# Kernel tuning notes

Measured on AMD Instinct MI355X. Metric: run time of the kernel, lower is better.

## Reference

```python
import jax, jax.numpy as jnp
import numpy as np


def setup_inputs() -> dict:
    key = jax.random.key(0)
    k1, k2, k3 = jax.random.split(key, 3)
    B, D, F = 4096, 1024, 16384  # batch, input_dim, dict_size
    x = jax.random.normal(k1, (B, D), dtype=jnp.float32)
    W_enc = jax.random.normal(k2, (F, D), dtype=jnp.float32) * (1.0 / np.sqrt(D))
    b_enc = jnp.zeros((F,), dtype=jnp.float32)
    W_dec = jax.random.normal(k3, (D, F), dtype=jnp.float32)
    # decoder columns are unit-normalized (as in _normalize_decoder)
    W_dec = W_dec / jnp.clip(jnp.linalg.norm(W_dec, axis=0, keepdims=True), 1e-8)
    b_dec = jnp.zeros((D,), dtype=jnp.float32)
    return {"x": x, "W_enc": W_enc, "b_enc": b_enc, "W_dec": W_dec, "b_dec": b_dec, "k": 32}


def reference(x, W_enc, b_enc, W_dec, b_dec, k):
    # encode: z_pre = (x - b_dec) @ W_enc^T + b_enc   -> [B, F]
    x_centered = x - b_dec
    z_pre = jnp.einsum('bd,fd->bf', x_centered, W_enc) + b_enc
    # activate: TopK(ReLU(z_pre)) via top_k + relu + scatter
    topk_vals, topk_idx = jax.lax.top_k(z_pre, k)           # [B, k]
    B = z_pre.shape[0]
    rows = jnp.arange(B)[:, None]                            # [B, 1]
    z = jnp.zeros_like(z_pre).at[rows, topk_idx].set(jax.nn.relu(topk_vals))
    # decode: x_hat = z @ W_dec^T + b_dec (dense matmul over sparse z)
    x_hat = jnp.einsum('bf,df->bd', z, W_dec) + b_dec
    return (x_hat, z, z_pre)
```

## Files before the change

kernel.cpp:

```cpp
#include <hip/hip_runtime.h>
#include <cstdint>
#include <cfloat>
#include <cstddef>

#define MAXK 128

typedef __attribute__((ext_vector_type(8))) short bf16x8;
typedef __attribute__((ext_vector_type(4))) float f32x4;

__device__ __forceinline__ void split8(const float4& v0, const float4& v1,
                                       uint4& hp, uint4& lp)
{
    float vv[8] = {v0.x, v0.y, v0.z, v0.w, v1.x, v1.y, v1.z, v1.w};
    unsigned h[8], l[8];
    #pragma unroll
    for (int i = 0; i < 8; ++i) {
        unsigned u  = __float_as_uint(vv[i]);
        unsigned hb = u & 0xFFFF0000u;
        float lf    = vv[i] - __uint_as_float(hb);
        h[i] = u;
        l[i] = __float_as_uint(lf);
    }
    hp.x = (h[0] >> 16) | (h[1] & 0xFFFF0000u);
    hp.y = (h[2] >> 16) | (h[3] & 0xFFFF0000u);
    hp.z = (h[4] >> 16) | (h[5] & 0xFFFF0000u);
    hp.w = (h[6] >> 16) | (h[7] & 0xFFFF0000u);
    lp.x = (l[0] >> 16) | (l[1] & 0xFFFF0000u);
    lp.y = (l[2] >> 16) | (l[3] & 0xFFFF0000u);
    lp.z = (l[4] >> 16) | (l[5] & 0xFFFF0000u);
    lp.w = (l[6] >> 16) | (l[7] & 0xFFFF0000u);
}

__device__ __forceinline__ void gload_lds16(const void* g, void* l)
{
    __builtin_amdgcn_global_load_lds(
        (const __attribute__((address_space(1))) unsigned int*)g,
        (__attribute__((address_space(3))) unsigned int*)l,
        16, 0, 0);
}

__global__ __launch_bounds__(256)
void prep_x_kernel(const float* __restrict__ x, const float* __restrict__ b_dec,
                   ushort* __restrict__ AhiP, ushort* __restrict__ AloP, int D)
{
    const int c   = blockIdx.x * 256 + threadIdx.x;
    const int t   = c >> 9;
    const int wc  = c & 511;
    const int rl  = wc >> 2;
    const int pkc = wc & 3;
    const int kc  = (pkc - (rl >> 1)) & 3;
    const int nkb = D >> 5;
    const int band = t / nkb, kblk = t - band * nkb;
    const int row = band * 128 + rl;
    const int k0  = kblk * 32 + kc * 8;

    const float* src = x + (size_t)row * D + k0;
    float4 v0 = *(const float4*)(src);
    float4 v1 = *(const float4*)(src + 4);
    const float* bd = b_dec + k0;
    float4 d0 = *(const float4*)(bd);
    float4 d1 = *(const float4*)(bd + 4);
    v0.x -= d0.x; v0.y -= d0.y; v0.z -= d0.z; v0.w -= d0.w;
    v1.x -= d1.x; v1.y -= d1.y; v1.z -= d1.z; v1.w -= d1.w;
    uint4 hp, lp;
    split8(v0, v1, hp, lp);
    const size_t off = (size_t)t * 4096 + (size_t)wc * 8;
    *(uint4*)&AhiP[off] = hp;
    *(uint4*)&AloP[off] = lp;
}

__global__ __launch_bounds__(256)
void prep_w_kernel(const float* __restrict__ Wenc,
                   ushort* __restrict__ WhiP, ushort* __restrict__ WloP, int D)
{
    const int c   = blockIdx.x * 256 + threadIdx.x;
    const int t   = c >> 10;
    const int wc  = c & 1023;
    const int rl  = wc >> 2;
    const int pkc = wc & 3;
    const int kc  = (pkc - (rl >> 1)) & 3;
    const int nkb = D >> 5;
    const int fband = t / nkb, kblk = t - fband * nkb;
    const int f   = fband * 256 + rl;
    const int k0  = kblk * 32 + kc * 8;

    const float* src = Wenc + (size_t)f * D + k0;
    float4 v0 = *(const float4*)(src);
    float4 v1 = *(const float4*)(src + 4);
    uint4 hp, lp;
    split8(v0, v1, hp, lp);
    const size_t off = (size_t)t * 8192 + (size_t)wc * 8;
    *(uint4*)&WhiP[off] = hp;
    *(uint4*)&WloP[off] = lp;
}

__global__ __launch_bounds__(256, 2)
void encode_gemm_pre(const ushort* __restrict__ AhiP, const ushort* __restrict__ AloP,
                     const ushort* __restrict__ WhiP, const ushort* __restrict__ WloP,
                     const float* __restrict__ b_enc, float* __restrict__ z_pre,
                     int D, int F)
{
    __shared__ ushort AsHi[4096];
    __shared__ ushort AsLo[4096];
    __shared__ ushort BsHi[2][8192];
    __shared__ ushort BsLo[2][8192];

    const int tid = threadIdx.x;
    const int bm  = blockIdx.y * 128;
    const int bn  = blockIdx.x * 256;

    const int lane = tid & 63;
    const int w    = tid >> 6;
    const int wm   = (w >> 1) * 64;
    const int wn   = (w & 1) * 128;
    const int fr   = lane & 15;
    const int q    = lane >> 4;
    const int nkb  = D >> 5;

    int aoff[4], boff[8];
    #pragma unroll
    for (int mi = 0; mi < 4; ++mi) {
        const int r = wm + mi * 16 + fr;
        aoff[mi] = r * 32 + (((q + (r >> 1)) & 3) * 8);
    }
    #pragma unroll
    for (int ni = 0; ni < 8; ++ni) {
        const int r = wn + ni * 16 + fr;
        boff[ni] = r * 32 + (((q + (r >> 1)) & 3) * 8);
    }

    f32x4 acc[4][8];
    #pragma unroll
    for (int mi = 0; mi < 4; ++mi)
        #pragma unroll
        for (int ni = 0; ni < 8; ++ni)
            acc[mi][ni] = (f32x4){0.f, 0.f, 0.f, 0.f};

    const char* aHi = (const char*)AhiP + (size_t)blockIdx.y * nkb * 8192;
    const char* aLo = (const char*)AloP + (size_t)blockIdx.y * nkb * 8192;
    const char* bHi = (const char*)WhiP + (size_t)blockIdx.x * nkb * 16384;
    const char* bLo = (const char*)WloP + (size_t)blockIdx.x * nkb * 16384;
    const int la16 = lane * 16;

    auto stageA = [&](int kb) {
        const char* pa = aHi + (size_t)kb * 8192;
        const char* pl = aLo + (size_t)kb * 8192;
        #pragma unroll
        for (int c = 0; c < 2; ++c) {
            const int off = (w * 2 + c) * 1024;
            gload_lds16(pa + off + la16, (char*)AsHi + off);
            gload_lds16(pl + off + la16, (char*)AsLo + off);
        }
    };
    auto stageB = [&](int kb, int buf) {
        const char* pb = bHi + (size_t)kb * 16384;
        const char* pm = bLo + (size_t)kb * 16384;
        #pragma unroll
        for (int c = 0; c < 4; ++c) {
            const int off = (w * 4 + c) * 1024;
            gload_lds16(pb + off + la16, (char*)&BsHi[buf][0] + off);
            gload_lds16(pm + off + la16, (char*)&BsLo[buf][0] + off);
        }
    };

    stageA(0);
    stageB(0, 0);
    asm volatile("s_waitcnt vmcnt(0)" ::: "memory");
    __syncthreads();

    int cur = 0;
    for (int kb = 0; kb < nkb; ++kb) {
        bf16x8 ahi[4], alo[4];
        #pragma unroll
        for (int mi = 0; mi < 4; ++mi) {
            ahi[mi] = *(const bf16x8*)&AsHi[aoff[mi]];
            alo[mi] = *(const bf16x8*)&AsLo[aoff[mi]];
        }
        __syncthreads();
        if (kb + 1 < nkb) {
            stageA(kb + 1);
            stageB(kb + 1, cur ^ 1);
        }
        const ushort* sBH = &BsHi[cur][0];
        const ushort* sBL = &BsLo[cur][0];
        #pragma unroll
        for (int ni = 0; ni < 8; ++ni) {
            bf16x8 bhi = *(const bf16x8*)&sBH[boff[ni]];
            bf16x8 blo = *(const bf16x8*)&sBL[boff[ni]];
            #pragma unroll
            for (int mi = 0; mi < 4; ++mi) {
                acc[mi][ni] = __builtin_amdgcn_mfma_f32_16x16x32_bf16(alo[mi], bhi, acc[mi][ni], 0, 0, 0);
                acc[mi][ni] = __builtin_amdgcn_mfma_f32_16x16x32_bf16(ahi[mi], blo, acc[mi][ni], 0, 0, 0);
                acc[mi][ni] = __builtin_amdgcn_mfma_f32_16x16x32_bf16(ahi[mi], bhi, acc[mi][ni], 0, 0, 0);
            }
        }
        asm volatile("s_waitcnt vmcnt(0)" ::: "memory");
        __syncthreads();
        cur ^= 1;
    }

    #pragma unroll
    for (int ni = 0; ni < 8; ++ni) {
        const int col = bn + wn + ni * 16 + fr;
        const float be = b_enc[col];
        #pragma unroll
        for (int mi = 0; mi < 4; ++mi) {
            const int rbase = bm + wm + mi * 16 + q * 4;
            float* dst = z_pre + (size_t)rbase * F + col;
            #pragma unroll
            for (int r = 0; r < 4; ++r)
                dst[(size_t)r * F] = acc[mi][ni][r] + be;
        }
    }
}

__global__ __launch_bounds__(256, 2)
void encode_gemm_bf16x3(const float* __restrict__ x, const float* __restrict__ Wenc,
                        const float* __restrict__ b_enc, const float* __restrict__ b_dec,
                        float* __restrict__ z_pre, int D, int F)
{
    constexpr int BM = 128, BN = 256, BK = 32;
    __shared__ ushort AsHi[BM * BK];
    __shared__ ushort AsLo[BM * BK];
    __shared__ ushort BsHi[BN * BK];
    __shared__ ushort BsLo[BN * BK];

    const int tid = threadIdx.x;
    const int bm  = blockIdx.y * BM;
    const int bn  = blockIdx.x * BN;

    const int lane = tid & 63;
    const int w    = tid >> 6;
    const int wm   = (w >> 1) * 64;
    const int wn   = (w & 1) * 128;
    const int fr   = lane & 15;
    const int q    = lane >> 4;

    int aoff[4], boff[8];
    #pragma unroll
    for (int mi = 0; mi < 4; ++mi) {
        const int r = wm + mi * 16 + fr;
        aoff[mi] = r * 32 + (((q + (r >> 1)) & 3) * 8);
    }
    #pragma unroll
    for (int ni = 0; ni < 8; ++ni) {
        const int r = wn + ni * 16 + fr;
        boff[ni] = r * 32 + (((q + (r >> 1)) & 3) * 8);
    }

    f32x4 acc[4][8];
    #pragma unroll
    for (int mi = 0; mi < 4; ++mi)
        #pragma unroll
        for (int ni = 0; ni < 8; ++ni)
            acc[mi][ni] = (f32x4){0.f, 0.f, 0.f, 0.f};

    for (int k0 = 0; k0 < D; k0 += BK) {
        #pragma unroll
        for (int j = 0; j < 2; ++j) {
            const int task = tid + 256 * j;
            const int row = task >> 2, kc = task & 3;
            const float* src = x + (size_t)(bm + row) * D + k0 + kc * 8;
            float4 v0 = *(const float4*)(src);
            float4 v1 = *(const float4*)(src + 4);
            const float* bd = b_dec + k0 + kc * 8;
            float4 d0 = *(const float4*)(bd);
            float4 d1 = *(const float4*)(bd + 4);
            v0.x -= d0.x; v0.y -= d0.y; v0.z -= d0.z; v0.w -= d0.w;
            v1.x -= d1.x; v1.y -= d1.y; v1.z -= d1.z; v1.w -= d1.w;
            uint4 hp, lp;
            split8(v0, v1, hp, lp);
            const int off = row * 32 + (((kc + (row >> 1)) & 3) * 8);
            *(uint4*)&AsHi[off] = hp;
            *(uint4*)&AsLo[off] = lp;
        }
        #pragma unroll
        for (int j = 0; j < 4; ++j) {
            const int task = tid + 256 * j;
            const int row = task >> 2, kc = task & 3;
            const float* src = Wenc + (size_t)(bn + row) * D + k0 + kc * 8;
            float4 v0 = *(const float4*)(src);
            float4 v1 = *(const float4*)(src + 4);
            uint4 hp, lp;
            split8(v0, v1, hp, lp);
            const int off = row * 32 + (((kc + (row >> 1)) & 3) * 8);
            *(uint4*)&BsHi[off] = hp;
            *(uint4*)&BsLo[off] = lp;
        }
        __syncthreads();

        bf16x8 ahi[4], alo[4];
        #pragma unroll
        for (int mi = 0; mi < 4; ++mi) {
            ahi[mi] = *(const bf16x8*)&AsHi[aoff[mi]];
            alo[mi] = *(const bf16x8*)&AsLo[aoff[mi]];
        }
        #pragma unroll
        for (int ni = 0; ni < 8; ++ni) {
            bf16x8 bhi = *(const bf16x8*)&BsHi[boff[ni]];
            bf16x8 blo = *(const bf16x8*)&BsLo[boff[ni]];
            #pragma unroll
            for (int mi = 0; mi < 4; ++mi) {
                acc[mi][ni] = __builtin_amdgcn_mfma_f32_16x16x32_bf16(alo[mi], bhi, acc[mi][ni], 0, 0, 0);
                acc[mi][ni] = __builtin_amdgcn_mfma_f32_16x16x32_bf16(ahi[mi], blo, acc[mi][ni], 0, 0, 0);
                acc[mi][ni] = __builtin_amdgcn_mfma_f32_16x16x32_bf16(ahi[mi], bhi, acc[mi][ni], 0, 0, 0);
            }
        }
        __syncthreads();
    }

    #pragma unroll
    for (int ni = 0; ni < 8; ++ni) {
        const int col = bn + wn + ni * 16 + fr;
        const float be = b_enc[col];
        #pragma unroll
        for (int mi = 0; mi < 4; ++mi) {
            const int rbase = bm + wm + mi * 16 + q * 4;
            float* dst = z_pre + (size_t)rbase * F + col;
            #pragma unroll
            for (int r = 0; r < 4; ++r)
                dst[(size_t)r * F] = acc[mi][ni][r] + be;
        }
    }
}

__device__ __forceinline__ unsigned fkey(float f)
{
    unsigned u = __float_as_uint(f);
    return u ^ ((unsigned)((int)u >> 31) | 0x80000000u);
}
__device__ __forceinline__ float finv(unsigned k)
{
    unsigned u = (k & 0x80000000u) ? (k ^ 0x80000000u) : ~k;
    return __uint_as_float(u);
}

__device__ __forceinline__ float exact_zpre(const float* __restrict__ xr,
                                            const float* __restrict__ Wenc,
                                            const float* __restrict__ b_enc,
                                            const float* __restrict__ b_dec,
                                            int f, int D, int ln)
{
    const float* wr = Wenc + (size_t)f * D;
    float s = 0.f;
    for (int d = ln * 4; d < D; d += 256) {
        float4 xv = *(const float4*)(xr + d);
        float4 bd = *(const float4*)(b_dec + d);
        float4 wv4 = *(const float4*)(wr + d);
        s = fmaf(xv.x - bd.x, wv4.x, s);
        s = fmaf(xv.y - bd.y, wv4.y, s);
        s = fmaf(xv.z - bd.z, wv4.z, s);
        s = fmaf(xv.w - bd.w, wv4.w, s);
    }
    #pragma unroll
    for (int o = 32; o > 0; o >>= 1) s += __shfl_down(s, o, 64);
    return s + b_enc[f];
}

#define DLT 4e-3f

template <int NVEC>
__global__ __launch_bounds__(256)
void topk_fast(const float* __restrict__ z_pre, float* __restrict__ z,
               float* __restrict__ ws_vals, int* __restrict__ ws_idx,
               const int* __restrict__ k_ptr,
               const float* __restrict__ x, const float* __restrict__ Wenc,
               const float* __restrict__ b_enc, const float* __restrict__ b_dec,
               int F, int D)
{
    const int row = blockIdx.x;
    const int t   = threadIdx.x;
    const int k   = *k_ptr;
    const int nv4 = F >> 2;
    const int wv_id = t >> 6, ln = t & 63;

    __shared__ ushort keys[16384];
    __shared__ float  cand_v[256];
    __shared__ int    cand_i[256];
    __shared__ unsigned char cand_sel[256];
    __shared__ int    bnd[128];
    __shared__ float  s2w[4];
    __shared__ int    hist4[4][256];
    __shared__ int    waveTot[4];
    __shared__ int    s_bin, s_above;
    __shared__ int    n_c_s, n_b_s, c_hi_s, out_cnt, cnt_tau_s, bad_s;
    __shared__ unsigned vk_key;

    if (t == 0) {
        n_c_s = 0; n_b_s = 0; c_hi_s = 0; out_cnt = 0; cnt_tau_s = 0; bad_s = 0;
        vk_key = 0xFFFFFFFFu;
    }

    const float*  zrow = z_pre + (size_t)row * F;
    const float4* src  = (const float4*)zrow;
    float4* dstz = (float4*)(z + (size_t)row * F);
    const float4 zz = make_float4(0.f, 0.f, 0.f, 0.f);

    float s2 = 0.f;
    #pragma unroll
    for (int i = 0; i < NVEC; ++i) {
        const int p = t + 256 * i;
        if (p < nv4) {
            const float4 v = src[p];
            dstz[p] = zz;
            const unsigned k0 = fkey(v.x) >> 16;
            const unsigned k1 = fkey(v.y) >> 16;
            const unsigned k2 = fkey(v.z) >> 16;
            const unsigned k3 = fkey(v.w) >> 16;
            uint2 pk;
            pk.x = k0 | (k1 << 16);
            pk.y = k2 | (k3 << 16);
            *(uint2*)&keys[p * 4] = pk;
            s2 = fmaf(v.x, v.x, s2);
            s2 = fmaf(v.y, v.y, s2);
            s2 = fmaf(v.z, v.z, s2);
            s2 = fmaf(v.w, v.w, s2);
        }
    }
    #pragma unroll
    for (int o = 32; o > 0; o >>= 1) s2 += __shfl_down(s2, o, 64);
    if (ln == 0) s2w[wv_id] = s2;
    __syncthreads();

    const float sigma = sqrtf((s2w[0] + s2w[1] + s2w[2] + s2w[3]) / (float)F);
    int c0 = 4 * k; if (c0 < 64) c0 = 64; if (c0 > 192) c0 = 192;
    const float qq  = (float)c0 / (float)F;
    const float tt  = sqrtf(-2.f * logf(qq));
    const float phi = tt - (2.30753f + 0.27061f * tt) /
                           (1.f + 0.99229f * tt + 0.04481f * tt * tt);
    const float tau = sigma * phi;
    const unsigned tk = fkey(tau) >> 16;
    const unsigned tkey16 = (tk >= 2) ? (tk - 2) : 0;

    const int nU = nv4 * 2;
    const unsigned* keysU = (const unsigned*)keys;
    for (int j = t; j < nU; j += 256) {
        const unsigned pr = keysU[j];
        const unsigned ka = pr & 0xFFFFu, kb = pr >> 16;
        if (ka > tkey16) { const int s = atomicAdd(&n_c_s, 1); if (s < 256) cand_i[s] = 2 * j; }
        if (kb > tkey16) { const int s = atomicAdd(&n_c_s, 1); if (s < 256) cand_i[s] = 2 * j + 1; }
    }
    __syncthreads();

    if (t == 0 && (n_c_s > 256 || !(tau > 0.1f))) bad_s = 1;
    const int n_c = min(n_c_s, 256);

    float myv = 0.f;
    if (t < n_c) {
        myv = zrow[cand_i[t]];
        cand_v[t] = myv;
        if (myv > tau) atomicAdd(&cnt_tau_s, 1);
    }
    __syncthreads();
    if (t == 0 && cnt_tau_s < k) bad_s = 1;

    cand_sel[t] = 0;
    if (t < n_c) {
        int gt = 0;
        for (int j = 0; j < n_c; ++j) gt += (cand_v[j] > myv);
        if (gt <= k - 1) atomicMin(&vk_key, fkey(myv));
    }
    __syncthreads();

    const float vkv = finv(vk_key);
    if (t < n_c) {
        if (myv > vkv + DLT) {
            cand_sel[t] = 2;
            atomicAdd(&c_hi_s, 1);
        } else if (myv > vkv - DLT) {
            const int sb = atomicAdd(&n_b_s, 1);
            if (sb < 128) bnd[sb] = t;
        }
    }
    __syncthreads();
    if (t == 0 && n_b_s > 128) bad_s = 1;
    __syncthreads();

    if (!bad_s) {
        const int n_b = n_b_s;
        const float* xr = x + (size_t)row * D;
        for (int b2 = wv_id; b2 < n_b; b2 += 4) {
            const int c = bnd[b2];
            const float ex = exact_zpre(xr, Wenc, b_enc, b_dec, cand_i[c], D, ln);
            if (ln == 0) cand_v[c] = ex;
        }
        __syncthreads();

        if (t == 0) {
            int need = k - c_hi_s;
            if (need > n_b) need = n_b;
            for (int it = 0; it < need; ++it) {
                int bi = -1; float bv = 0.f;
                for (int b2 = 0; b2 < n_b; ++b2) {
                    const int c = bnd[b2];
                    if (cand_sel[c]) continue;
                    const float v = cand_v[c];
                    if (bi < 0 || v > bv || (v == bv && cand_i[c] < cand_i[bi])) {
                        bi = c; bv = v;
                    }
                }
                if (bi < 0) break;
                cand_sel[bi] = 1;
            }
        }
        __syncthreads();

        float* wvp = ws_vals + (size_t)row * MAXK;
        int*   wip = ws_idx  + (size_t)row * MAXK;
        if (t < n_c && cand_sel[t]) {
            const float zv = fmaxf(cand_v[t], 0.f);
            z[(size_t)row * F + cand_i[t]] = zv;
            const int s = atomicAdd(&out_cnt, 1);
            if (s < MAXK) { wvp[s] = zv; wip[s] = cand_i[t]; }
        }
        return;
    }

    if (t == 0) { n_c_s = 0; c_hi_s = 0; out_cnt = 0; }
    __syncthreads();

    unsigned prefix = 0;
    int rem = k;
    for (int pass = 0; pass < 2; ++pass) {
        const int shift = 24 - 8 * pass;
        hist4[0][t] = 0; hist4[1][t] = 0; hist4[2][t] = 0; hist4[3][t] = 0;
        __syncthreads();
        for (int j = t; j < F; j += 256) {
            const unsigned key = fkey(zrow[j]);
            const bool inb = (pass == 0) || ((key >> (shift + 8)) == prefix);
            if (inb) atomicAdd(&hist4[wv_id][(key >> shift) & 255], 1);
        }
        __syncthreads();
        const int cnt = hist4[0][t] + hist4[1][t] + hist4[2][t] + hist4[3][t];
        int s = cnt;
        #pragma unroll
        for (int off = 1; off < 64; off <<= 1) {
            const int tmp = __shfl_down(s, off, 64);
            if (ln + off < 64) s += tmp;
        }
        if (ln == 0) waveTot[wv_id] = s;
        __syncthreads();
        int add = 0;
        #pragma unroll
        for (int w2 = 0; w2 < 4; ++w2)
            if (w2 > wv_id) add += waveTot[w2];
        const int sfx = s + add;
        const int nxt = sfx - cnt;
        if (sfx >= rem && nxt < rem) { s_bin = t; s_above = nxt; }
        __syncthreads();
        rem -= s_above;
        prefix = (prefix << 8) | (unsigned)s_bin;
        __syncthreads();
    }

    const float hiT = finv((prefix << 16) | 0xFFFFu) + DLT;
    const float loT = finv(prefix << 16) - DLT;

    for (int j = t; j < F; j += 256) {
        const float v = zrow[j];
        if (v > hiT) atomicAdd(&c_hi_s, 1);
        else if (v > loT) {
            const int s = atomicAdd(&n_c_s, 1);
            if (s < 256) { cand_i[s] = j; cand_sel[s] = 0; }
        }
    }
    __syncthreads();
    const int n_c2 = min(n_c_s, 256);

    {
        const float* xr = x + (size_t)row * D;
        for (int c = wv_id; c < n_c2; c += 4) {
            const float ex = exact_zpre(xr, Wenc, b_enc, b_dec, cand_i[c], D, ln);
            if (ln == 0) cand_v[c] = ex;
        }
    }
    __syncthreads();

    if (t == 0) {
        int need = k - c_hi_s;
        if (need > n_c2) need = n_c2;
        for (int it = 0; it < need; ++it) {
            int bi = -1; float bv = 0.f;
            for (int c = 0; c < n_c2; ++c) {
                if (cand_sel[c]) continue;
                const float v = cand_v[c];
                if (bi < 0 || v > bv || (v == bv && cand_i[c] < cand_i[bi])) {
                    bi = c; bv = v;
                }
            }
            if (bi < 0) break;
            cand_sel[bi] = 1;
        }
    }
    __syncthreads();

    {
        const float4 z4 = make_float4(0.f, 0.f, 0.f, 0.f);
        #pragma unroll
        for (int i = 0; i < NVEC; ++i) {
            const int p = t + 256 * i;
            if (p < nv4) dstz[p] = z4;
        }
    }
    __syncthreads();

    float* wvp = ws_vals + (size_t)row * MAXK;
    int*   wip = ws_idx  + (size_t)row * MAXK;
    for (int j = t; j < F; j += 256) {
        const float v = zrow[j];
        if (v > hiT) {
            const float zv = fmaxf(v, 0.f);
            z[(size_t)row * F + j] = zv;
            const int s = atomicAdd(&out_cnt, 1);
            if (s < MAXK) { wvp[s] = zv; wip[s] = j; }
        }
    }
    if (t < n_c2 && cand_sel[t]) {
        const float zv = fmaxf(cand_v[t], 0.f);
        z[(size_t)row * F + cand_i[t]] = zv;
        const int s = atomicAdd(&out_cnt, 1);
        if (s < MAXK) { wvp[s] = zv; wip[s] = cand_i[t]; }
    }
}

template <int NVEC>
__global__ __launch_bounds__(256)
void topk_kernel(const float* __restrict__ z_pre, float* __restrict__ z,
                 float* __restrict__ ws_vals, int* __restrict__ ws_idx,
                 const int* __restrict__ k_ptr,
                 const float* __restrict__ x, const float* __restrict__ Wenc,
                 const float* __restrict__ b_enc, const float* __restrict__ b_dec,
                 int F, int D)
{
    const int row = blockIdx.x;
    const int t   = threadIdx.x;
    const int k   = *k_ptr;
    const int nv4 = F >> 2;
    const int wv_id = t >> 6;
    const int ln    = t & 63;

    const float4* src = (const float4*)(z_pre + (size_t)row * F);
    float4 vals[NVEC];
    #pragma unroll
    for (int i = 0; i < NVEC; ++i) {
        const int p = t + 256 * i;
        if (p < nv4) vals[i] = src[p];
        else         vals[i] = make_float4(-FLT_MAX, -FLT_MAX, -FLT_MAX, -FLT_MAX);
    }

    __shared__ int hist[4][256];
    __shared__ int waveTot[4];
    __shared__ int s_bin, s_above;
    __shared__ int c_hi_s, n_c_s, out_cnt;
    __shared__ int cand_idx[128];
    __shared__ float cand_val[128];
    __shared__ unsigned char cand_sel[128];

    unsigned prefix = 0;
    int rem = k;

    #pragma unroll
    for (int pass = 0; pass < 2; ++pass) {
        const int shift = 24 - 8 * pass;
        hist[0][t] = 0; hist[1][t] = 0; hist[2][t] = 0; hist[3][t] = 0;
        __syncthreads();
        #pragma unroll
        for (int i = 0; i < NVEC; ++i) {
            const float* vv = (const float*)&vals[i];
            #pragma unroll
            for (int j = 0; j < 4; ++j) {
                const unsigned key = fkey(vv[j]);
                const bool inb = (pass == 0) || ((key >> (shift + 8)) == prefix);
                if (inb) atomicAdd(&hist[wv_id][(key >> shift) & 255], 1);
            }
        }
        __syncthreads();
        const int cnt = hist[0][t] + hist[1][t] + hist[2][t] + hist[3][t];
        int s = cnt;
        #pragma unroll
        for (int off = 1; off < 64; off <<= 1) {
            const int tmp = __shfl_down(s, off, 64);
            if (ln + off < 64) s += tmp;
        }
        if (ln == 0) waveTot[wv_id] = s;
        __syncthreads();
        int add = 0;
        #pragma unroll
        for (int w2 = 0; w2 < 4; ++w2)
            if (w2 > wv_id) add += waveTot[w2];
        const int sfx = s + add;
        const int nxt = sfx - cnt;
        if (sfx >= rem && nxt < rem) { s_bin = t; s_above = nxt; }
        __syncthreads();
        rem -= s_above;
        prefix = (prefix << 8) | (unsigned)s_bin;
        __syncthreads();
    }

    const unsigned keyLo = prefix << 16;
    const unsigned keyHi = keyLo | 0xFFFFu;
    const float dlt = 1e-3f;
    const float hiThr = finv(keyHi) + dlt;
    const float loThr = finv(keyLo) - dlt;

    if (t == 0) { c_hi_s = 0; n_c_s = 0; out_cnt = 0; }
    __syncthreads();

    #pragma unroll
    for (int i = 0; i < NVEC; ++i) {
        const float* vv = (const float*)&vals[i];
        #pragma unroll
        for (int j = 0; j < 4; ++j) {
            const float v = vv[j];
            if (v > hiThr) {
                atomicAdd(&c_hi_s, 1);
            } else if (v > loThr) {
                const int s = atomicAdd(&n_c_s, 1);
                if (s < 128) { cand_idx[s] = (t + 256 * i) * 4 + j; cand_sel[s] = 0; }
            }
        }
    }
    __syncthreads();

    const int n_c = min(n_c_s, 128);

    {
        const float* xr = x + (size_t)row * D;
        for (int c = wv_id; c < n_c; c += 4) {
            const float ex = exact_zpre(xr, Wenc, b_enc, b_dec, cand_idx[c], D, ln);
            if (ln == 0) cand_val[c] = ex;
        }
    }
    __syncthreads();

    if (t == 0) {
        int need = k - c_hi_s;
        if (need > n_c) need = n_c;
        for (int it = 0; it < need; ++it) {
            int bi = -1; float bv = 0.f;
            for (int c = 0; c < n_c; ++c) {
                if (cand_sel[c]) continue;
                const float v = cand_val[c];
                if (bi < 0 || v > bv || (v == bv && cand_idx[c] < cand_idx[bi])) {
                    bi = c; bv = v;
                }
            }
            if (bi < 0) break;
            cand_sel[bi] = 1;
        }
    }
    __syncthreads();

    float4* dstz = (float4*)(z + (size_t)row * F);
    float*  wv   = ws_vals + (size_t)row * MAXK;
    int*    wi   = ws_idx  + (size_t)row * MAXK;

    #pragma unroll
    for (int i = 0; i < NVEC; ++i) {
        const int p4 = t + 256 * i;
        if (p4 < nv4) {
            const float* vv = (const float*)&vals[i];
            float4 outv;
            float* ov = (float*)&outv;
            #pragma unroll
            for (int j = 0; j < 4; ++j) {
                const int pos = p4 * 4 + j;
                const float v = vv[j];
                float zv = 0.f;
                bool sel = false;
                if (v > hiThr) {
                    zv = fmaxf(v, 0.f); sel = true;
                } else if (v > loThr) {
                    for (int c = 0; c < n_c; ++c) {
                        if (cand_idx[c] == pos) {
                            if (cand_sel[c]) { zv = fmaxf(cand_val[c], 0.f); sel = true; }
                            break;
                        }
                    }
                }
                ov[j] = zv;
                if (sel) {
                    const int s = atomicAdd(&out_cnt, 1);
                    if (s < MAXK) { wv[s] = zv; wi[s] = pos; }
                }
            }
            dstz[p4] = outv;
        }
    }
}

__global__ __launch_bounds__(256)
void transpose4_kernel(const float* __restrict__ in, float* __restrict__ out,
                       int R, int C)
{
    __shared__ float tile[64][65];
    const int c0 = blockIdx.x * 64;
    const int r0 = blockIdx.y * 64;
    const int t  = threadIdx.x;
    const int tc = (t & 15) * 4;
    const int tr = t >> 4;

    #pragma unroll
    for (int i = 0; i < 4; ++i) {
        const int r = tr + i * 16;
        const float4 v = *(const float4*)(in + (size_t)(r0 + r) * C + c0 + tc);
        tile[r][tc]     = v.x;
        tile[r][tc + 1] = v.y;
        tile[r][tc + 2] = v.z;
        tile[r][tc + 3] = v.w;
    }
    __syncthreads();
    #pragma unroll
    for (int i = 0; i < 4; ++i) {
        const int c = tr + i * 16;
        float4 v;
        v.x = tile[tc]    [c];
        v.y = tile[tc + 1][c];
        v.z = tile[tc + 2][c];
        v.w = tile[tc + 3][c];
        *(float4*)(out + (size_t)(c0 + c) * R + r0 + tc) = v;
    }
}

__global__ __launch_bounds__(256)
void transpose_kernel(const float* __restrict__ in, float* __restrict__ out,
                      int R, int C)
{
    __shared__ float tile[32][33];
    const int c0 = blockIdx.x * 32;
    const int r0 = blockIdx.y * 32;
    const int tx = threadIdx.x & 31;
    const int ty = threadIdx.x >> 5;

    #pragma unroll
    for (int i = ty; i < 32; i += 8) {
        const int r = r0 + i, c = c0 + tx;
        tile[i][tx] = (r < R && c < C) ? in[(size_t)r * C + c] : 0.f;
    }
    __syncthreads();
    #pragma unroll
    for (int i = ty; i < 32; i += 8) {
        const int c = c0 + i, r = r0 + tx;
        if (c < C && r < R) out[(size_t)c * R + r] = tile[tx][i];
    }
}

__global__ __launch_bounds__(256)
void decode_kernel(const float* __restrict__ WdT, const float* __restrict__ wvals,
                   const int* __restrict__ widx, const float* __restrict__ b_dec,
                   float* __restrict__ x_hat, const int* __restrict__ k_ptr, int D)
{
    __shared__ float sv[MAXK];
    __shared__ int   si[MAXK];
    const int row = blockIdx.x;
    const int t   = threadIdx.x;
    int k = *k_ptr;
    if (k > MAXK) k = MAXK;

    if (t < MAXK) {
        sv[t] = wvals[(size_t)row * MAXK + t];
        si[t] = widx [(size_t)row * MAXK + t];
    }
    __syncthreads();

    for (int d0 = t * 4; d0 < D; d0 += 1024) {
        float4 a0 = *(const float4*)(b_dec + d0);
        float4 a1 = make_float4(0.f, 0.f, 0.f, 0.f);
        float4 a2 = make_float4(0.f, 0.f, 0.f, 0.f);
        float4 a3 = make_float4(0.f, 0.f, 0.f, 0.f);
        int j = 0;
        for (; j + 4 <= k; j += 4) {
            const float v0 = sv[j], v1 = sv[j+1], v2 = sv[j+2], v3 = sv[j+3];
            const float4 w0 = *(const float4*)(WdT + (size_t)si[j]   * D + d0);
            const float4 w1 = *(const float4*)(WdT + (size_t)si[j+1] * D + d0);
            const float4 w2 = *(const float4*)(WdT + (size_t)si[j+2] * D + d0);
            const float4 w3 = *(const float4*)(WdT + (size_t)si[j+3] * D + d0);
            a0.x = fmaf(v0, w0.x, a0.x); a0.y = fmaf(v0, w0.y, a0.y);
            a0.z = fmaf(v0, w0.z, a0.z); a0.w = fmaf(v0, w0.w, a0.w);
            a1.x = fmaf(v1, w1.x, a1.x); a1.y = fmaf(v1, w1.y, a1.y);
            a1.z = fmaf(v1, w1.z, a1.z); a1.w = fmaf(v1, w1.w, a1.w);
            a2.x = fmaf(v2, w2.x, a2.x); a2.y = fmaf(v2, w2.y, a2.y);
            a2.z = fmaf(v2, w2.z, a2.z); a2.w = fmaf(v2, w2.w, a2.w);
            a3.x = fmaf(v3, w3.x, a3.x); a3.y = fmaf(v3, w3.y, a3.y);
            a3.z = fmaf(v3, w3.z, a3.z); a3.w = fmaf(v3, w3.w, a3.w);
        }
        for (; j < k; ++j) {
            const float v0 = sv[j];
            const float4 w0 = *(const float4*)(WdT + (size_t)si[j] * D + d0);
            a0.x = fmaf(v0, w0.x, a0.x); a0.y = fmaf(v0, w0.y, a0.y);
            a0.z = fmaf(v0, w0.z, a0.z); a0.w = fmaf(v0, w0.w, a0.w);
        }
        a0.x += a1.x + a2.x + a3.x;
        a0.y += a1.y + a2.y + a3.y;
        a0.z += a1.z + a2.z + a3.z;
        a0.w += a1.w + a2.w + a3.w;
        *(float4*)(x_hat + (size_t)row * D + d0) = a0;
    }
}

extern "C" void kernel_launch(void* const* d_in, const int* in_sizes, int n_in,
                              void* d_out, int out_size, void* d_ws, size_t ws_size,
                              hipStream_t stream)
{
    const float* x     = (const float*)d_in[0];
    const float* W_enc = (const float*)d_in[1];
    const float* b_enc = (const float*)d_in[2];
    const float* W_dec = (const float*)d_in[3];
    const float* b_dec = (const float*)d_in[4];
    const int*   k_ptr = (const int*)d_in[5];

    const int F = in_sizes[2];
    const int D = in_sizes[4];
    const int B = in_sizes[0] / D;

    float* x_hat = (float*)d_out;
    float* z     = x_hat + (size_t)B * D;
    float* z_pre = z + (size_t)B * F;

    float* WdT = (float*)d_ws;
    float* wv  = WdT + (size_t)F * D;
    int*   wi  = (int*)(wv + (size_t)B * MAXK);
    char*  extra = (char*)(wi + (size_t)B * MAXK);

    const size_t base_need  = (size_t)F * D * 4 + (size_t)B * MAXK * 8;
    const size_t extra_need = (size_t)B * D * 4 + (size_t)F * D * 4;
    const bool use_pre = (ws_size >= base_need + extra_need) &&
                         (D % 32 == 0) && (B % 128 == 0) && (F % 256 == 0);

    if (use_pre) {
        ushort* AhiP = (ushort*)extra;
        ushort* AloP = AhiP + (size_t)B * D;
        ushort* WhiP = AloP + (size_t)B * D;
        ushort* WloP = WhiP + (size_t)F * D;

        prep_x_kernel<<<(B * (D / 8)) / 256, 256, 0, stream>>>(x, b_dec, AhiP, AloP, D);
        prep_w_kernel<<<(F * (D / 8)) / 256, 256, 0, stream>>>(W_enc, WhiP, WloP, D);
        encode_gemm_pre<<<dim3(F / 256, B / 128), 256, 0, stream>>>(
            AhiP, AloP, WhiP, WloP, b_enc, z_pre, D, F);
    } else {
        encode_gemm_bf16x3<<<dim3(F / 256, B / 128), 256, 0, stream>>>(
            x, W_enc, b_enc, b_dec, z_pre, D, F);
    }

    if ((D % 64 == 0) && (F % 64 == 0)) {
        transpose4_kernel<<<dim3(F / 64, D / 64), 256, 0, stream>>>(
            W_dec, WdT, D, F);
    } else {
        transpose_kernel<<<dim3((F + 31) / 32, (D + 31) / 32), 256, 0, stream>>>(
            W_dec, WdT, D, F);
    }

    const int nv4  = F / 4;
    const int nvec = (nv4 + 255) / 256;
    const bool fastok = (F <= 16384) && ((F & 3) == 0);

    if (fastok) {
        if (nvec <= 4)
            topk_fast<4><<<B, 256, 0, stream>>>(z_pre, z, wv, wi, k_ptr, x, W_enc, b_enc, b_dec, F, D);
        else if (nvec <= 8)
            topk_fast<8><<<B, 256, 0, stream>>>(z_pre, z, wv, wi, k_ptr, x, W_enc, b_enc, b_dec, F, D);
        else
            topk_fast<16><<<B, 256, 0, stream>>>(z_pre, z, wv, wi, k_ptr, x, W_enc, b_enc, b_dec, F, D);
    } else {
        if (nvec <= 8)
            topk_kernel<8><<<B, 256, 0, stream>>>(z_pre, z, wv, wi, k_ptr, x, W_enc, b_enc, b_dec, F, D);
        else if (nvec <= 16)
            topk_kernel<16><<<B, 256, 0, stream>>>(z_pre, z, wv, wi, k_ptr, x, W_enc, b_enc, b_dec, F, D);
        else
            topk_kernel<32><<<B, 256, 0, stream>>>(z_pre, z, wv, wi, k_ptr, x, W_enc, b_enc, b_dec, F, D);
    }

    decode_kernel<<<B, 256, 0, stream>>>(WdT, wv, wi, b_dec, x_hat, k_ptr, D);
}
```

Before: 1.109 ms.

## Filter top-k candidates in the GEMM epilogue using a per-row Gaussian threshold

A new per-row kernel estimates a threshold from the row's norm and a Gaussian quantile approximation. The encode GEMM epilogue then appends every value above a lower threshold to a small per-row candidate buffer using atomics. The top-k kernel works only on those candidates: it finds the k-th value, recomputes near-boundary entries exactly, and falls back to a full radix pass over z_pre when the candidate set is too large or too small. z is zeroed by a separate fill kernel, so the top-k kernel no longer reads the whole z_pre row. The cost is global atomics in the GEMM epilogue and a separate zero-fill pass.

Result: slower. 1.210 ms (+9.2%).

```diff
diff --git a/kernel.cpp b/kernel.cpp
--- a/kernel.cpp
+++ b/kernel.cpp
@@ -4,6 +4,8 @@
 #include <cstddef>
 
 #define MAXK 128
+#define FCAP 256
+#define DLT 4e-3f
 
 typedef __attribute__((ext_vector_type(8))) short bf16x8;
 typedef __attribute__((ext_vector_type(4))) float f32x4;
@@ -37,6 +39,39 @@
         (const __attribute__((address_space(1))) unsigned int*)g,
         (__attribute__((address_space(3))) unsigned int*)l,
         16, 0, 0);
+}
+
+__device__ __forceinline__ unsigned fkey(float f)
+{
+    unsigned u = __float_as_uint(f);
+    return u ^ ((unsigned)((int)u >> 31) | 0x80000000u);
+}
+__device__ __forceinline__ float finv(unsigned k)
+{
+    unsigned u = (k & 0x80000000u) ? (k ^ 0x80000000u) : ~k;
+    return __uint_as_float(u);
+}
+
+__device__ __forceinline__ float exact_zpre(const float* __restrict__ xr,
+                                            const float* __restrict__ Wenc,
+                                            const float* __restrict__ b_enc,
+                                            const float* __restrict__ b_dec,
+                                            int f, int D, int ln)
+{
+    const float* wr = Wenc + (size_t)f * D;
+    float s = 0.f;
+    for (int d = ln * 4; d < D; d += 256) {
+        float4 xv = *(const float4*)(xr + d);
+        float4 bd = *(const float4*)(b_dec + d);
+        float4 wv4 = *(const float4*)(wr + d);
+        s = fmaf(xv.x - bd.x, wv4.x, s);
+        s = fmaf(xv.y - bd.y, wv4.y, s);
+        s = fmaf(xv.z - bd.z, wv4.z, s);
+        s = fmaf(xv.w - bd.w, wv4.w, s);
+    }
+    #pragma unroll
+    for (int o = 32; o > 0; o >>= 1) s += __shfl_down(s, o, 64);
+    return s + b_enc[f];
 }
 
 __global__ __launch_bounds__(256)
@@ -94,11 +129,66 @@
     *(uint4*)&WloP[off] = lp;
 }
 
+__global__ __launch_bounds__(256)
+void tau_kernel(const float* __restrict__ x, const float* __restrict__ b_dec,
+                const int* __restrict__ k_ptr,
+                float* __restrict__ tau_arr, float* __restrict__ taulo_arr,
+                int* __restrict__ ccnt, int F, int D)
+{
+    const int row = blockIdx.x, t = threadIdx.x;
+    const int wv_id = t >> 6, ln = t & 63;
+    __shared__ float s2w[4];
+
+    float s2 = 0.f;
+    for (int d = t * 4; d < D; d += 1024) {
+        float4 xv = *(const float4*)(x + (size_t)row * D + d);
+        float4 bd = *(const float4*)(b_dec + d);
+        const float a = xv.x - bd.x, b = xv.y - bd.y;
+        const float c = xv.z - bd.z, e = xv.w - bd.w;
+        s2 = fmaf(a, a, s2); s2 = fmaf(b, b, s2);
+        s2 = fmaf(c, c, s2); s2 = fmaf(e, e, s2);
+    }
+    #pragma unroll
+    for (int o = 32; o > 0; o >>= 1) s2 += __shfl_down(s2, o, 64);
+    if (ln == 0) s2w[wv_id] = s2;
+    __syncthreads();
+
+    if (t == 0) {
+        const int k = *k_ptr;
+        const float sig = sqrtf((s2w[0] + s2w[1] + s2w[2] + s2w[3]) / (float)D);
+        float tau, taulo;
+        if (k <= 40 && F >= 4096 && sig > 1e-4f) {
+            const float qq  = 160.f / (float)F;
+            const float tt  = sqrtf(-2.f * logf(qq));
+            const float phi = tt - (2.30753f + 0.27061f * tt) /
+                                   (1.f + 0.99229f * tt + 0.04481f * tt * tt);
+            tau   = sig * phi;
+            taulo = tau - 0.03f * sig;
+        } else {
+            tau = -1.f; taulo = FLT_MAX;
+        }
+        tau_arr[row]   = tau;
+        taulo_arr[row] = taulo;
+        ccnt[row]      = 0;
+    }
+}
+
+__global__ __launch_bounds__(256)
+void zfill_kernel(float4* __restrict__ p, long n4)
+{
+    const float4 zz = make_float4(0.f, 0.f, 0.f, 0.f);
+    const long stride = (long)gridDim.x * 256;
+    for (long i = (long)blockIdx.x * 256 + threadIdx.x; i < n4; i += stride)
+        p[i] = zz;
+}
+
 __global__ __launch_bounds__(256, 2)
-void encode_gemm_pre(const ushort* __restrict__ AhiP, const ushort* __restrict__ AloP,
-                     const ushort* __restrict__ WhiP, const ushort* __restrict__ WloP,
-                     const float* __restrict__ b_enc, float* __restrict__ z_pre,
-                     int D, int F)
+void encode_gemm_filter(const ushort* __restrict__ AhiP, const ushort* __restrict__ AloP,
+                        const ushort* __restrict__ WhiP, const ushort* __restrict__ WloP,
+                        const float* __restrict__ b_enc, float* __restrict__ z_pre,
+                        const float* __restrict__ taulo_arr,
+                        int* __restrict__ ccnt, float* __restrict__ cvalB,
+                        int* __restrict__ cidxB, int D, int F)
 {
     __shared__ ushort AsHi[4096];
     __shared__ ushort AsLo[4096];
@@ -197,6 +287,332 @@
         asm volatile("s_waitcnt vmcnt(0)" ::: "memory");
         __syncthreads();
         cur ^= 1;
+    }
+
+    float tlo[4][4];
+    #pragma unroll
+    for (int mi = 0; mi < 4; ++mi)
+        #pragma unroll
+        for (int r = 0; r < 4; ++r)
+            tlo[mi][r] = taulo_arr[bm + wm + mi * 16 + q * 4 + r];
+
+    #pragma unroll
+    for (int ni = 0; ni < 8; ++ni) {
+        const int col = bn + wn + ni * 16 + fr;
+        const float be = b_enc[col];
+        #pragma unroll
+        for (int mi = 0; mi < 4; ++mi) {
+            const int rbase = bm + wm + mi * 16 + q * 4;
+            float* dst = z_pre + (size_t)rbase * F + col;
+            #pragma unroll
+            for (int r = 0; r < 4; ++r) {
+                const float val = acc[mi][ni][r] + be;
+                dst[(size_t)r * F] = val;
+                if (val > tlo[mi][r]) {
+                    const int rowi = rbase + r;
+                    const int s = atomicAdd(&ccnt[rowi], 1);
+                    if (s < FCAP) {
+                        cvalB[(size_t)rowi * FCAP + s] = val;
+                        cidxB[(size_t)rowi * FCAP + s] = col;
+                    }
+                }
+            }
+        }
+    }
+}
+
+__global__ __launch_bounds__(256)
+void topk_select(const float* __restrict__ z_pre, float* __restrict__ z,
+                 float* __restrict__ ws_vals, int* __restrict__ ws_idx,
+                 const int* __restrict__ k_ptr,
+                 const float* __restrict__ x, const float* __restrict__ Wenc,
+                 const float* __restrict__ b_enc, const float* __restrict__ b_dec,
+                 const float* __restrict__ tau_arr, const int* __restrict__ ccnt,
+                 const float* __restrict__ cvalB, const int* __restrict__ cidxB,
+                 int F, int D)
+{
+    const int row = blockIdx.x;
+    const int t   = threadIdx.x;
+    const int k   = *k_ptr;
+    const int wv_id = t >> 6, ln = t & 63;
+
+    __shared__ float cand_v[FCAP];
+    __shared__ int   cand_i[FCAP];
+    __shared__ unsigned char cand_sel[FCAP];
+    __shared__ int   bnd[128];
+    __shared__ int   hist4[4][256];
+    __shared__ int   waveTot[4];
+    __shared__ int   s_bin, s_above;
+    __shared__ int   n_b_s, c_hi_s, out_cnt, cnt_tau_s, bad_s, n_c_s;
+    __shared__ unsigned vk_key;
+
+    if (t == 0) {
+        n_b_s = 0; c_hi_s = 0; out_cnt = 0; cnt_tau_s = 0; bad_s = 0;
+        vk_key = 0xFFFFFFFFu;
+    }
+    __syncthreads();
+
+    const float tau = tau_arr[row];
+    const int cnt   = ccnt[row];
+    if (t == 0 && (cnt > FCAP || !(tau > 0.1f))) bad_s = 1;
+    const int n_c = min(cnt, FCAP);
+
+    const float* zrow = z_pre + (size_t)row * F;
+    float* wvp = ws_vals + (size_t)row * MAXK;
+    int*   wip = ws_idx  + (size_t)row * MAXK;
+
+    float myv = -FLT_MAX;
+    cand_sel[t] = 0;
+    if (t < n_c) {
+        myv = cvalB[(size_t)row * FCAP + t];
+        cand_v[t] = myv;
+        cand_i[t] = cidxB[(size_t)row * FCAP + t];
+        if (myv > tau) atomicAdd(&cnt_tau_s, 1);
+    }
+    __syncthreads();
+    if (t == 0 && cnt_tau_s < k) bad_s = 1;
+
+    if (t < n_c) {
+        int gt = 0;
+        for (int j = 0; j < n_c; ++j) gt += (cand_v[j] > myv);
+        if (gt <= k - 1) atomicMin(&vk_key, fkey(myv));
+    }
+    __syncthreads();
+
+    const float vkv = finv(vk_key);
+    if (t < n_c) {
+        if (myv > vkv + DLT) {
+            cand_sel[t] = 2;
+            atomicAdd(&c_hi_s, 1);
+        } else if (myv > vkv - DLT) {
+            const int sb = atomicAdd(&n_b_s, 1);
+            if (sb < 128) bnd[sb] = t;
+        }
+    }
+    __syncthreads();
+    if (t == 0 && n_b_s > 128) bad_s = 1;
+    __syncthreads();
+
+    if (!bad_s) {
+        const int n_b = n_b_s;
+        const float* xr = x + (size_t)row * D;
+        for (int b2 = wv_id; b2 < n_b; b2 += 4) {
+            const int c = bnd[b2];
+            const float ex = exact_zpre(xr, Wenc, b_enc, b_dec, cand_i[c], D, ln);
+            if (ln == 0) cand_v[c] = ex;
+        }
+        __syncthreads();
+
+        if (t == 0) {
+            int need = k - c_hi_s;
+            if (need > n_b) need = n_b;
+            for (int it = 0; it < need; ++it) {
+                int bi = -1; float bv = 0.f;
+                for (int b2 = 0; b2 < n_b; ++b2) {
+                    const int c = bnd[b2];
+                    if (cand_sel[c]) continue;
+                    const float v = cand_v[c];
+                    if (bi < 0 || v > bv || (v == bv && cand_i[c] < cand_i[bi])) {
+                        bi = c; bv = v;
+                    }
+                }
+                if (bi < 0) break;
+                cand_sel[bi] = 1;
+            }
+        }
+        __syncthreads();
+
+        if (t < n_c && cand_sel[t]) {
+            const float zv = fmaxf(cand_v[t], 0.f);
+            z[(size_t)row * F + cand_i[t]] = zv;
+            const int s = atomicAdd(&out_cnt, 1);
+            if (s < MAXK) { wvp[s] = zv; wip[s] = cand_i[t]; }
+        }
+        return;
+    }
+
+    if (t == 0) { n_c_s = 0; c_hi_s = 0; out_cnt = 0; }
+    __syncthreads();
+
+    unsigned prefix = 0;
+    int rem = k;
+    for (int pass = 0; pass < 2; ++pass) {
+        const int shift = 24 - 8 * pass;
+        hist4[0][t] = 0; hist4[1][t] = 0; hist4[2][t] = 0; hist4[3][t] = 0;
+        __syncthreads();
+        for (int j = t; j < F; j += 256) {
+            const unsigned key = fkey(zrow[j]);
+            const bool inb = (pass == 0) || ((key >> (shift + 8)) == prefix);
+            if (inb) atomicAdd(&hist4[wv_id][(key >> shift) & 255], 1);
+        }
+        __syncthreads();
+        const int cnt2 = hist4[0][t] + hist4[1][t] + hist4[2][t] + hist4[3][t];
+        int s = cnt2;
+        #pragma unroll
+        for (int off = 1; off < 64; off <<= 1) {
+            const int tmp = __shfl_down(s, off, 64);
+            if (ln + off < 64) s += tmp;
+        }
+        if (ln == 0) waveTot[wv_id] = s;
+        __syncthreads();
+        int add = 0;
+        #pragma unroll
+        for (int w2 = 0; w2 < 4; ++w2)
+            if (w2 > wv_id) add += waveTot[w2];
+        const int sfx = s + add;
+        const int nxt = sfx - cnt2;
+        if (sfx >= rem && nxt < rem) { s_bin = t; s_above = nxt; }
+        __syncthreads();
+        rem -= s_above;
+        prefix = (prefix << 8) | (unsigned)s_bin;
+        __syncthreads();
+    }
+
+    const float hiT = finv((prefix << 16) | 0xFFFFu) + DLT;
+    const float loT = finv(prefix << 16) - DLT;
+
+    for (int j = t; j < F; j += 256) {
+        const float v = zrow[j];
+        if (v > hiT) atomicAdd(&c_hi_s, 1);
+        else if (v > loT) {
+            const int s = atomicAdd(&n_c_s, 1);
+            if (s < FCAP) { cand_i[s] = j; cand_sel[s] = 0; }
+        }
+    }
+    __syncthreads();
+    const int n_c2 = min(n_c_s, FCAP);
+
+    {
+        const float* xr = x + (size_t)row * D;
+        for (int c = wv_id; c < n_c2; c += 4) {
+            const float ex = exact_zpre(xr, Wenc, b_enc, b_dec, cand_i[c], D, ln);
+            if (ln == 0) cand_v[c] = ex;
+        }
+    }
+    __syncthreads();
+
+    if (t == 0) {
+        int need = k - c_hi_s;
+        if (need > n_c2) need = n_c2;
+        for (int it = 0; it < need; ++it) {
+            int bi = -1; float bv = 0.f;
+            for (int c = 0; c < n_c2; ++c) {
+                if (cand_sel[c]) continue;
+                const float v = cand_v[c];
+                if (bi < 0 || v > bv || (v == bv && cand_i[c] < cand_i[bi])) {
+                    bi = c; bv = v;
+                }
+            }
+            if (bi < 0) break;
+            cand_sel[bi] = 1;
+        }
+    }
+    __syncthreads();
+
+    for (int j = t; j < F; j += 256) {
+        const float v = zrow[j];
+        if (v > hiT) {
+            const float zv = fmaxf(v, 0.f);
+            z[(size_t)row * F + j] = zv;
+            const int s = atomicAdd(&out_cnt, 1);
+            if (s < MAXK) { wvp[s] = zv; wip[s] = j; }
+        }
+    }
+    if (t < n_c2 && cand_sel[t]) {
+        const float zv = fmaxf(cand_v[t], 0.f);
+        z[(size_t)row * F + cand_i[t]] = zv;
+        const int s = atomicAdd(&out_cnt, 1);
+        if (s < MAXK) { wvp[s] = zv; wip[s] = cand_i[t]; }
+    }
+}
+
+__global__ __launch_bounds__(256, 2)
+void encode_gemm_pre(const ushort* __restrict__ AhiP, const ushort* __restrict__ AloP,
+                     const ushort* __restrict__ WhiP, const ushort* __restrict__ WloP,
+                     const float* __restrict__ b_enc, float* __restrict__ z_pre,
+                     int D, int F)
+{
+    __shared__ ushort AsHi[4096];
+    __shared__ ushort AsLo[4096];
+    __shared__ ushort BsHi[8192];
+    __shared__ ushort BsLo[8192];
+
+    const int tid = threadIdx.x;
+    const int bm  = blockIdx.y * 128;
+    const int bn  = blockIdx.x * 256;
+
+    const int lane = tid & 63;
+    const int w    = tid >> 6;
+    const int wm   = (w >> 1) * 64;
+    const int wn   = (w & 1) * 128;
+    const int fr   = lane & 15;
+    const int q    = lane >> 4;
+    const int nkb  = D >> 5;
+
+    int aoff[4], boff[8];
+    #pragma unroll
+    for (int mi = 0; mi < 4; ++mi) {
+        const int r = wm + mi * 16 + fr;
+        aoff[mi] = r * 32 + (((q + (r >> 1)) & 3) * 8);
+    }
+    #pragma unroll
+    for (int ni = 0; ni < 8; ++ni) {
+        const int r = wn + ni * 16 + fr;
+        boff[ni] = r * 32 + (((q + (r >> 1)) & 3) * 8);
+    }
+
+    f32x4 acc[4][8];
+    #pragma unroll
+    for (int mi = 0; mi < 4; ++mi)
+        #pragma unroll
+        for (int ni = 0; ni < 8; ++ni)
+            acc[mi][ni] = (f32x4){0.f, 0.f, 0.f, 0.f};
+
+    const char* aHi = (const char*)AhiP + (size_t)blockIdx.y * nkb * 8192;
+    const char* aLo = (const char*)AloP + (size_t)blockIdx.y * nkb * 8192;
+    const char* bHi = (const char*)WhiP + (size_t)blockIdx.x * nkb * 16384;
+    const char* bLo = (const char*)WloP + (size_t)blockIdx.x * nkb * 16384;
+    const int la16 = lane * 16;
+
+    for (int kb = 0; kb < nkb; ++kb) {
+        const char* pa = aHi + (size_t)kb * 8192;
+        const char* pl = aLo + (size_t)kb * 8192;
+        const char* pb = bHi + (size_t)kb * 16384;
+        const char* pm = bLo + (size_t)kb * 16384;
+
+        #pragma unroll
+        for (int c = 0; c < 2; ++c) {
+            const int off = (w * 2 + c) * 1024;
+            gload_lds16(pa + off + la16, (char*)AsHi + off);
+            gload_lds16(pl + off + la16, (char*)AsLo + off);
+        }
+        #pragma unroll
+        for (int c = 0; c < 4; ++c) {
+            const int off = (w * 4 + c) * 1024;
+            gload_lds16(pb + off + la16, (char*)BsHi + off);
+            gload_lds16(pm + off + la16, (char*)BsLo + off);
+        }
+        asm volatile("s_waitcnt vmcnt(0)" ::: "memory");
+        __syncthreads();
+
+        bf16x8 ahi[4], alo[4];
+        #pragma unroll
+        for (int mi = 0; mi < 4; ++mi) {
+            ahi[mi] = *(const bf16x8*)&AsHi[aoff[mi]];
+            alo[mi] = *(const bf16x8*)&AsLo[aoff[mi]];
+        }
+        #pragma unroll
+        for (int ni = 0; ni < 8; ++ni) {
+            bf16x8 bhi = *(const bf16x8*)&BsHi[boff[ni]];
+            bf16x8 blo = *(const bf16x8*)&BsLo[boff[ni]];
+            #pragma unroll
+            for (int mi = 0; mi < 4; ++mi) {
+                acc[mi][ni] = __builtin_amdgcn_mfma_f32_16x16x32_bf16(alo[mi], bhi, acc[mi][ni], 0, 0, 0);
+                acc[mi][ni] = __builtin_amdgcn_mfma_f32_16x16x32_bf16(ahi[mi], blo, acc[mi][ni], 0, 0, 0);
+                acc[mi][ni] = __builtin_amdgcn_mfma_f32_16x16x32_bf16(ahi[mi], bhi, acc[mi][ni], 0, 0, 0);
+            }
+        }
+        __syncthreads();
     }
 
     #pragma unroll
@@ -323,41 +739,6 @@
         }
     }
 }
-
-__device__ __forceinline__ unsigned fkey(float f)
-{
-    unsigned u = __float_as_uint(f);
-    return u ^ ((unsigned)((int)u >> 31) | 0x80000000u);
-}
-__device__ __forceinline__ float finv(unsigned k)
-{
-    unsigned u = (k & 0x80000000u) ? (k ^ 0x80000000u) : ~k;
-    return __uint_as_float(u);
-}
-
-__device__ __forceinline__ float exact_zpre(const float* __restrict__ xr,
-                                            const float* __restrict__ Wenc,
-                                            const float* __restrict__ b_enc,
-                                            const float* __restrict__ b_dec,
-                                            int f, int D, int ln)
-{
-    const float* wr = Wenc + (size_t)f * D;
-    float s = 0.f;
-    for (int d = ln * 4; d < D; d += 256) {
-        float4 xv = *(const float4*)(xr + d);
-        float4 bd = *(const float4*)(b_dec + d);
-        float4 wv4 = *(const float4*)(wr + d);
-        s = fmaf(xv.x - bd.x, wv4.x, s);
-        s = fmaf(xv.y - bd.y, wv4.y, s);
-        s = fmaf(xv.z - bd.z, wv4.z, s);
-        s = fmaf(xv.w - bd.w, wv4.w, s);
-    }
-    #pragma unroll
-    for (int o = 32; o > 0; o >>= 1) s += __shfl_down(s, o, 64);
-    return s + b_enc[f];
-}
-
-#define DLT 4e-3f
 
 template <int NVEC>
 __global__ __launch_bounds__(256)
@@ -620,172 +1001,6 @@
         z[(size_t)row * F + cand_i[t]] = zv;
         const int s = atomicAdd(&out_cnt, 1);
         if (s < MAXK) { wvp[s] = zv; wip[s] = cand_i[t]; }
-    }
-}
-
-template <int NVEC>
-__global__ __launch_bounds__(256)
-void topk_kernel(const float* __restrict__ z_pre, float* __restrict__ z,
-                 float* __restrict__ ws_vals, int* __restrict__ ws_idx,
-                 const int* __restrict__ k_ptr,
-                 const float* __restrict__ x, const float* __restrict__ Wenc,
-                 const float* __restrict__ b_enc, const float* __restrict__ b_dec,
-                 int F, int D)
-{
-    const int row = blockIdx.x;
-    const int t   = threadIdx.x;
-    const int k   = *k_ptr;
-    const int nv4 = F >> 2;
-    const int wv_id = t >> 6;
-    const int ln    = t & 63;
-
-    const float4* src = (const float4*)(z_pre + (size_t)row * F);
-    float4 vals[NVEC];
-    #pragma unroll
-    for (int i = 0; i < NVEC; ++i) {
-        const int p = t + 256 * i;
-        if (p < nv4) vals[i] = src[p];
-        else         vals[i] = make_float4(-FLT_MAX, -FLT_MAX, -FLT_MAX, -FLT_MAX);
-    }
-
-    __shared__ int hist[4][256];
-    __shared__ int waveTot[4];
-    __shared__ int s_bin, s_above;
-    __shared__ int c_hi_s, n_c_s, out_cnt;
-    __shared__ int cand_idx[128];
-    __shared__ float cand_val[128];
-    __shared__ unsigned char cand_sel[128];
-
-    unsigned prefix = 0;
-    int rem = k;
-
-    #pragma unroll
-    for (int pass = 0; pass < 2; ++pass) {
-        const int shift = 24 - 8 * pass;
-        hist[0][t] = 0; hist[1][t] = 0; hist[2][t] = 0; hist[3][t] = 0;
-        __syncthreads();
-        #pragma unroll
-        for (int i = 0; i < NVEC; ++i) {
-            const float* vv = (const float*)&vals[i];
-            #pragma unroll
-            for (int j = 0; j < 4; ++j) {
-                const unsigned key = fkey(vv[j]);
-                const bool inb = (pass == 0) || ((key >> (shift + 8)) == prefix);
-                if (inb) atomicAdd(&hist[wv_id][(key >> shift) & 255], 1);
-            }
-        }
-        __syncthreads();
-        const int cnt = hist[0][t] + hist[1][t] + hist[2][t] + hist[3][t];
-        int s = cnt;
-        #pragma unroll
-        for (int off = 1; off < 64; off <<= 1) {
-            const int tmp = __shfl_down(s, off, 64);
-            if (ln + off < 64) s += tmp;
-        }
-        if (ln == 0) waveTot[wv_id] = s;
-        __syncthreads();
-        int add = 0;
-        #pragma unroll
-        for (int w2 = 0; w2 < 4; ++w2)
-            if (w2 > wv_id) add += waveTot[w2];
-        const int sfx = s + add;
-        const int nxt = sfx - cnt;
-        if (sfx >= rem && nxt < rem) { s_bin = t; s_above = nxt; }
-        __syncthreads();
-        rem -= s_above;
-        prefix = (prefix << 8) | (unsigned)s_bin;
-        __syncthreads();
-    }
-
-    const unsigned keyLo = prefix << 16;
-    const unsigned keyHi = keyLo | 0xFFFFu;
-    const float dlt = 1e-3f;
-    const float hiThr = finv(keyHi) + dlt;
-    const float loThr = finv(keyLo) - dlt;
-
-    if (t == 0) { c_hi_s = 0; n_c_s = 0; out_cnt = 0; }
-    __syncthreads();
-
-    #pragma unroll
-    for (int i = 0; i < NVEC; ++i) {
-        const float* vv = (const float*)&vals[i];
-        #pragma unroll
-        for (int j = 0; j < 4; ++j) {
-            const float v = vv[j];
-            if (v > hiThr) {
-                atomicAdd(&c_hi_s, 1);
-            } else if (v > loThr) {
-                const int s = atomicAdd(&n_c_s, 1);
-                if (s < 128) { cand_idx[s] = (t + 256 * i) * 4 + j; cand_sel[s] = 0; }
-            }
-        }
-    }
-    __syncthreads();
-
-    const int n_c = min(n_c_s, 128);
-
-    {
-        const float* xr = x + (size_t)row * D;
-        for (int c = wv_id; c < n_c; c += 4) {
-            const float ex = exact_zpre(xr, Wenc, b_enc, b_dec, cand_idx[c], D, ln);
-            if (ln == 0) cand_val[c] = ex;
-        }
-    }
-    __syncthreads();
-
-    if (t == 0) {
-        int need = k - c_hi_s;
-        if (need > n_c) need = n_c;
-        for (int it = 0; it < need; ++it) {
-            int bi = -1; float bv = 0.f;
-            for (int c = 0; c < n_c; ++c) {
-                if (cand_sel[c]) continue;
-                const float v = cand_val[c];
-                if (bi < 0 || v > bv || (v == bv && cand_idx[c] < cand_idx[bi])) {
-                    bi = c; bv = v;
-                }
-            }
-            if (bi < 0) break;
-            cand_sel[bi] = 1;
-        }
-    }
-    __syncthreads();
-
-    float4* dstz = (float4*)(z + (size_t)row * F);
-    float*  wv   = ws_vals + (size_t)row * MAXK;
-    int*    wi   = ws_idx  + (size_t)row * MAXK;
-
-    #pragma unroll
-    for (int i = 0; i < NVEC; ++i) {
-        const int p4 = t + 256 * i;
-        if (p4 < nv4) {
-            const float* vv = (const float*)&vals[i];
-            float4 outv;
-            float* ov = (float*)&outv;
-            #pragma unroll
-            for (int j = 0; j < 4; ++j) {
-                const int pos = p4 * 4 + j;
-                const float v = vv[j];
-                float zv = 0.f;
-                bool sel = false;
-                if (v > hiThr) {
-                    zv = fmaxf(v, 0.f); sel = true;
-                } else if (v > loThr) {
-                    for (int c = 0; c < n_c; ++c) {
-                        if (cand_idx[c] == pos) {
-                            if (cand_sel[c]) { zv = fmaxf(cand_val[c], 0.f); sel = true; }
-                            break;
-                        }
-                    }
-                }
-                ov[j] = zv;
-                if (sel) {
-                    const int s = atomicAdd(&out_cnt, 1);
-                    if (s < MAXK) { wv[s] = zv; wi[s] = pos; }
-                }
-            }
-            dstz[p4] = outv;
-        }
     }
 }
 
@@ -922,10 +1137,14 @@
     int*   wi  = (int*)(wv + (size_t)B * MAXK);
     char*  extra = (char*)(wi + (size_t)B * MAXK);
 
-    const size_t base_need  = (size_t)F * D * 4 + (size_t)B * MAXK * 8;
-    const size_t extra_need = (size_t)B * D * 4 + (size_t)F * D * 4;
+    const size_t base_need   = (size_t)F * D * 4 + (size_t)B * MAXK * 8;
+    const size_t extra_need  = (size_t)B * D * 4 + (size_t)F * D * 4;
+    const size_t filter_need = (size_t)B * 12 + (size_t)B * FCAP * 8;
     const bool use_pre = (ws_size >= base_need + extra_need) &&
                          (D % 32 == 0) && (B % 128 == 0) && (F % 256 == 0);
+    const bool use_filter = use_pre &&
+                            (ws_size >= base_need + extra_need + filter_need) &&
+                            ((F & 3) == 0);
 
     if (use_pre) {
         ushort* AhiP = (ushort*)extra;
@@ -935,6 +1154,34 @@
 
         prep_x_kernel<<<(B * (D / 8)) / 256, 256, 0, stream>>>(x, b_dec, AhiP, AloP, D);
         prep_w_kernel<<<(F * (D / 8)) / 256, 256, 0, stream>>>(W_enc, WhiP, WloP, D);
+
+        if (use_filter) {
+            float* tau_arr   = (float*)(WloP + (size_t)F * D);
+            float* taulo_arr = tau_arr + B;
+            int*   ccnt      = (int*)(taulo_arr + B);
+            float* cvalB     = (float*)(ccnt + B);
+            int*   cidxB     = (int*)(cvalB + (size_t)B * FCAP);
+
+            tau_kernel<<<B, 256, 0, stream>>>(x, b_dec, k_ptr, tau_arr, taulo_arr,
+                                              ccnt, F, D);
+            encode_gemm_filter<<<dim3(F / 256, B / 128), 256, 0, stream>>>(
+                AhiP, AloP, WhiP, WloP, b_enc, z_pre, taulo_arr, ccnt, cvalB, cidxB, D, F);
+
+            if ((D % 64 == 0) && (F % 64 == 0))
+                transpose4_kernel<<<dim3(F / 64, D / 64), 256, 0, stream>>>(W_dec, WdT, D, F);
+            else
+                transpose_kernel<<<dim3((F + 31) / 32, (D + 31) / 32), 256, 0, stream>>>(W_dec, WdT, D, F);
+
+            const long n4 = (long)B * F / 4;
+            zfill_kernel<<<2048, 256, 0, stream>>>((float4*)z, n4);
+
+            topk_select<<<B, 256, 0, stream>>>(z_pre, z, wv, wi, k_ptr, x, W_enc,
+                                               b_enc, b_dec, tau_arr, ccnt, cvalB,
+                                               cidxB, F, D);
+            decode_kernel<<<B, 256, 0, stream>>>(WdT, wv, wi, b_dec, x_hat, k_ptr, D);
+            return;
+        }
+
         encode_gemm_pre<<<dim3(F / 256, B / 128), 256, 0, stream>>>(
             AhiP, AloP, WhiP, WloP, b_enc, z_pre, D, F);
     } else {
@@ -942,13 +1189,10 @@
             x, W_enc, b_enc, b_dec, z_pre, D, F);
     }
 
-    if ((D % 64 == 0) && (F % 64 == 0)) {
-        transpose4_kernel<<<dim3(F / 64, D / 64), 256, 0, stream>>>(
-            W_dec, WdT, D, F);
-    } else {
-        transpose_kernel<<<dim3((F + 31) / 32, (D + 31) / 32), 256, 0, stream>>>(
-            W_dec, WdT, D, F);
-    }
+    if ((D % 64 == 0) && (F % 64 == 0))
+        transpose4_kernel<<<dim3(F / 64, D / 64), 256, 0, stream>>>(W_dec, WdT, D, F);
+    else
+        transpose_kernel<<<dim3((F + 31) / 32, (D + 31) / 32), 256, 0, stream>>>(W_dec, WdT, D, F);
 
     const int nv4  = F / 4;
     const int nvec = (nv4 + 255) / 256;
@@ -962,12 +1206,7 @@
         else
             topk_fast<16><<<B, 256, 0, stream>>>(z_pre, z, wv, wi, k_ptr, x, W_enc, b_enc, b_dec, F, D);
     } else {
-        if (nvec <= 8)
-            topk_kernel<8><<<B, 256, 0, stream>>>(z_pre, z, wv, wi, k_ptr, x, W_enc, b_enc, b_dec, F, D);
-        else if (nvec <= 16)
-            topk_kernel<16><<<B, 256, 0, stream>>>(z_pre, z, wv, wi, k_ptr, x, W_enc, b_enc, b_dec, F, D);
-        else
-            topk_kernel<32><<<B, 256, 0, stream>>>(z_pre, z, wv, wi, k_ptr, x, W_enc, b_enc, b_dec, F, D);
+        topk_fast<16><<<B, 256, 0, stream>>>(z_pre, z, wv, wi, k_ptr, x, W_enc, b_enc, b_dec, F, D);
     }
 
     decode_kernel<<<B, 256, 0, stream>>>(WdT, wv, wi, b_dec, x_hat, k_ptr, D);
```
